# Optimization experiments

Measured on AMD Instinct MI355X. Metric: run time of the kernel, lower is better.

## Reference

```python
import jax, jax.numpy as jnp
import numpy as np
from jax import lax

B, S, D, F, T = 16, 1024, 256, 256, 8192
K = 3  # conv kernel size


def setup_inputs() -> dict:
    key = jax.random.key(0)
    ks = jax.random.split(key, 16)

    def conv_w(k, cin, cout):
        # kaiming-style, scaled down to keep exp(log_dur) in a sane range
        return jax.random.normal(k, (cout, cin, K), jnp.float32) * np.float32(np.sqrt(2.0 / (cin * K)) * 0.5)

    def lin_w(k, cin, cout, std=0.01):
        return jax.random.normal(k, (cin, cout), jnp.float32) * np.float32(std)

    inp = {
        "x": jax.random.normal(ks[0], (B, S, D), jnp.float32),
        "phone_masks": jnp.zeros((B, S), bool),
        "note_pitch": jax.random.normal(ks[1], (B, S, D), jnp.float32),
        # DurationPredictor (has extra LayerNorm)
        "ln_g": jnp.ones((D,), jnp.float32),
        "ln_b": jnp.zeros((D,), jnp.float32),
        "dp_w1": conv_w(ks[2], D, F), "dp_b1": jnp.full((F,), 0.1, jnp.float32),
        "dp_w2": conv_w(ks[3], F, F), "dp_b2": jnp.full((F,), 0.1, jnp.float32),
        "dp_wl": lin_w(ks[4], F, 1), "dp_bl": jnp.full((1,), 1.5, jnp.float32),
        # Pitch predictor (output_dim=3, bias [5.4, 1.7, 0.0])
        "pp_w1": conv_w(ks[5], D, F), "pp_b1": jnp.full((F,), 0.1, jnp.float32),
        "pp_w2": conv_w(ks[6], F, F), "pp_b2": jnp.full((F,), 0.1, jnp.float32),
        "pp_wl": lin_w(ks[7], F, 3), "pp_bl": jnp.array([5.4, 1.7, 0.0], jnp.float32),
        # Energy predictor (output_dim=1, bias 1.0)
        "ep_w1": conv_w(ks[8], D, F), "ep_b1": jnp.full((F,), 0.1, jnp.float32),
        "ep_w2": conv_w(ks[9], F, F), "ep_b2": jnp.full((F,), 0.1, jnp.float32),
        "ep_wl": lin_w(ks[10], F, 1), "ep_bl": jnp.full((1,), 1.0, jnp.float32),
        # note projection Linear(D, D)
        "np_w": lin_w(ks[11], D, D, std=1.0 / np.sqrt(D)),
        "np_b": jnp.zeros((D,), jnp.float32),
        "max_length": T,
    }
    return inp


def _conv1d(h, w, b):
    # h: [B, C, S], w: [O, C, K] -> [B, O, S], SAME padding (torch padding=(K-1)//2)
    y = lax.conv_general_dilated(h, w, (1,), "SAME", dimension_numbers=("NCH", "OIH", "NCH"))
    return y + b[None, :, None]


def _predictor(x, mask, w1, b1, w2, b2, wl, bl):
    # SimpleVariancePredictor.forward (dropout = eval-mode identity)
    h = jnp.swapaxes(x, 1, 2)                       # [B, C, S]
    h = jax.nn.relu(_conv1d(h, w1, b1))
    h = jax.nn.relu(_conv1d(h, w2, b2))
    out = jnp.swapaxes(h, 1, 2) @ wl + bl           # [B, S, out_dim]
    return jnp.where(mask[..., None], 0.0, out)


def _layernorm(x, g, b, eps=1e-5):
    m = jnp.mean(x, axis=-1, keepdims=True)
    v = jnp.mean(jnp.square(x - m), axis=-1, keepdims=True)
    return g * (x - m) * lax.rsqrt(v + eps) + b


def _duration_predictor(x, mask, ln_g, ln_b, w1, b1, w2, b2, wl, bl):
    xn = _layernorm(x, ln_g, ln_b)
    phoneme_energy = jnp.linalg.norm(xn, axis=2, keepdims=True)     # [B, S, 1]
    base = _predictor(xn, mask, w1, b1, w2, b2, wl, bl)
    energy_scale = 0.8 + 0.4 * (phoneme_energy / jnp.max(phoneme_energy))
    seq_len = x.shape[1]
    pos = jnp.arange(seq_len, dtype=x.dtype)[None, :, None]
    pos_scale = 1.0 + 0.1 * (pos / seq_len)
    out = base * energy_scale * pos_scale
    return jnp.where(mask[..., None], 0.0, out)


def _length_regulate(x, durations, max_length):
    # x: [B, S, C], durations: [B, S] float -> expanded [B, T, C], mel_masks [B, T]
    d = jnp.round(durations).astype(jnp.int32)
    cum = jnp.cumsum(d, axis=1)
    # _limit_durations: clip cumsum at max_length == reduce overflow token, zero the rest
    cumc = jnp.minimum(cum, max_length)
    t = jnp.arange(max_length, dtype=jnp.int32)
    # frame t belongs to phoneme j with cumc[j-1] <= t < cumc[j]  (parallel prefix-sum indexing)
    idx = jax.vmap(lambda c: jnp.searchsorted(c, t, side="right"))(cumc)   # [B, T]
    mel_masks = t[None, :] >= cumc[:, -1:]
    seq_len = x.shape[1]
    expanded = jnp.take_along_axis(x, jnp.clip(idx, 0, seq_len - 1)[:, :, None], axis=1)
    expanded = jnp.where(mel_masks[:, :, None], 0.0, expanded)
    return expanded, mel_masks


def reference(x, phone_masks, note_pitch, ln_g, ln_b,
              dp_w1, dp_b1, dp_w2, dp_b2, dp_wl, dp_bl,
              pp_w1, pp_b1, pp_w2, pp_b2, pp_wl, pp_bl,
              ep_w1, ep_b1, ep_w2, ep_b2, ep_wl, ep_bl,
              np_w, np_b, max_length):
    tempo_factor = 1.0
    x = x + (note_pitch @ np_w + np_b)

    log_durations = _duration_predictor(x, phone_masks, ln_g, ln_b,
                                        dp_w1, dp_b1, dp_w2, dp_b2, dp_wl, dp_bl)
    durations = jnp.exp(log_durations) * tempo_factor               # [B, S, 1]

    pitch_params = _predictor(x, phone_masks, pp_w1, pp_b1, pp_w2, pp_b2, pp_wl, pp_bl)  # [B, S, 3]
    phoneme_energy = jnp.linalg.norm(x, axis=2, keepdims=True)
    energy_norm = (phoneme_energy - jnp.min(phoneme_energy)) / (
        jnp.max(phoneme_energy) - jnp.min(phoneme_energy) + 1e-8)
    f0_scale = 100.0 + 400.0 * jnp.squeeze(energy_norm, -1)          # [B, S]
    f0_base = jnp.exp(pitch_params[:, :, 0]) * f0_scale / 220.0
    modified_f0 = jnp.log(f0_base + 1e-8)
    pitch_params = jnp.concatenate([modified_f0[..., None], pitch_params[:, :, 1:]], axis=2)

    energy = _predictor(x, phone_masks, ep_w1, ep_b1, ep_w2, ep_b2, ep_wl, ep_bl)        # [B, S, 1]

    expanded_features, mel_masks = _length_regulate(x, jnp.squeeze(durations, -1), max_length)
    return log_durations, durations, pitch_params, energy, expanded_features, mel_masks
```

## Files before the change

### kernel.cpp

```cpp
#include <hip/hip_runtime.h>
#include <math.h>

#define B_ 16
#define S_ 1024
#define D_ 256
#define F_ 256
#define T_ 8192
#define ROWS (B_ * S_)

typedef __attribute__((ext_vector_type(8))) short short8x;
typedef __attribute__((ext_vector_type(4))) float f32x4;

static __device__ __forceinline__ unsigned short f2bf(float f) {
    unsigned u = __float_as_uint(f);
    unsigned r = (u + 0x7FFFu + ((u >> 16) & 1u)) >> 16;
    return (unsigned short)r;
}
static __device__ __forceinline__ float bf2f(unsigned short h) {
    return __uint_as_float(((unsigned)h) << 16);
}

__global__ __launch_bounds__(256) void wprep_kernel(
    const float* __restrict__ pw1, const float* __restrict__ ew1,
    const float* __restrict__ pw2, const float* __restrict__ ew2,
    const float* __restrict__ dw1, const float* __restrict__ dw2,
    unsigned short* __restrict__ wt)
{
    int idx = blockIdx.x * 256 + threadIdx.x;
    int o = idx >> 8, c = idx & 255;
    int o_t = o >> 6, nt = (o >> 4) & 3, lr = o & 15;
    int cbk = c >> 5, hs = (c >> 3) & 3, j = c & 7;
    int lane = hs * 16 + lr;
    size_t fbase = ((size_t)o_t * 8 + cbk) * 3;

    const float* srcs[4] = { pw1, ew1, pw2, ew2 };
    #pragma unroll
    for (int t = 0; t < 4; ++t) {
        const float* p = srcs[t] + ((size_t)o * 256 + c) * 3;
        unsigned short* dst = wt + (size_t)t * 196608;
        #pragma unroll
        for (int k = 0; k < 3; ++k) {
            size_t off = (((fbase + k) * 4 + nt) * 64 + lane) * 8 + j;
            dst[off] = f2bf(p[k]);
        }
    }
    const float* dsrc[2] = { dw1, dw2 };
    #pragma unroll
    for (int t = 0; t < 2; ++t) {
        const float* p = dsrc[t] + ((size_t)o * 256 + c) * 3;
        unsigned short* dh = wt + (size_t)(4 + 2 * t) * 196608;
        unsigned short* dl = dh + 196608;
        #pragma unroll
        for (int k = 0; k < 3; ++k) {
            size_t off = (((fbase + k) * 4 + nt) * 64 + lane) * 8 + j;
            float v = p[k];
            unsigned short hi = f2bf(v);
            dh[off] = hi;
            dl[off] = f2bf(v - bf2f(hi));
        }
    }
}

__global__ __launch_bounds__(256) void noteproj_kernel(
    const float* __restrict__ x, const float* __restrict__ note,
    const float* __restrict__ w, const float* __restrict__ bias,
    float* __restrict__ xp, unsigned* __restrict__ red)
{
    if (blockIdx.x == 0 && blockIdx.y == 0 && threadIdx.x == 0) {
        red[0] = 0u;
        red[1] = 0x7F7FFFFFu;
        red[2] = 0u;
    }
    __shared__ float As[16][66];
    __shared__ float Bs[16][68];
    const int tid = threadIdx.x;
    const int m0 = blockIdx.x << 6;
    const int o0 = blockIdx.y << 6;
    const int tc = tid & 15, tr = tid >> 4;
    const int r = tr << 2, oc = tc << 2;
    const int tA = tid >> 2, cg = (tid & 3) << 2;
    const int cB = tid >> 4, oB = (tid & 15) << 2;
    float acc[4][4] = {};

    for (int c0 = 0; c0 < D_; c0 += 16) {
        float4 av = *(const float4*)(note + (size_t)(m0 + tA) * D_ + c0 + cg);
        As[cg + 0][tA] = av.x; As[cg + 1][tA] = av.y;
        As[cg + 2][tA] = av.z; As[cg + 3][tA] = av.w;
        *(float4*)&Bs[cB][oB] = *(const float4*)(w + (size_t)(c0 + cB) * D_ + o0 + oB);
        __syncthreads();
        #pragma unroll
        for (int c = 0; c < 16; ++c) {
            float a[4], bv[4];
            #pragma unroll
            for (int m = 0; m < 4; ++m) a[m] = As[c][r + m];
            #pragma unroll
            for (int j = 0; j < 4; ++j) bv[j] = Bs[c][oc + j];
            #pragma unroll
            for (int i = 0; i < 4; ++i)
                #pragma unroll
                for (int j = 0; j < 4; ++j)
                    acc[i][j] = fmaf(a[i], bv[j], acc[i][j]);
        }
        __syncthreads();
    }
    #pragma unroll
    for (int i = 0; i < 4; ++i) {
        size_t row = (size_t)(m0 + r + i);
        const float* xr = x + row * D_ + o0 + oc;
        float4 v;
        v.x = acc[i][0] + bias[o0 + oc + 0] + xr[0];
        v.y = acc[i][1] + bias[o0 + oc + 1] + xr[1];
        v.z = acc[i][2] + bias[o0 + oc + 2] + xr[2];
        v.w = acc[i][3] + bias[o0 + oc + 3] + xr[3];
        *(float4*)(xp + row * D_ + o0 + oc) = v;
    }
}

__global__ __launch_bounds__(256) void rowstats_kernel(
    const float* __restrict__ xp, const float* __restrict__ g, const float* __restrict__ bb,
    unsigned short* __restrict__ xnh, unsigned short* __restrict__ xnl,
    float* __restrict__ nxn, float* __restrict__ nx,
    unsigned short* __restrict__ xpb)
{
    int row = blockIdx.x * 4 + (threadIdx.x >> 6);
    int lane = threadIdx.x & 63;
    float4 v = ((const float4*)(xp + (size_t)row * D_))[lane];
    ushort4 bv4;
    bv4.x = f2bf(v.x); bv4.y = f2bf(v.y); bv4.z = f2bf(v.z); bv4.w = f2bf(v.w);
    ((ushort4*)xpb)[(size_t)row * 64 + lane] = bv4;

    float s = v.x + v.y + v.z + v.w;
    float sq = v.x * v.x + v.y * v.y + v.z * v.z + v.w * v.w;
    #pragma unroll
    for (int m = 32; m; m >>= 1) { s += __shfl_xor(s, m); sq += __shfl_xor(sq, m); }
    float mean = s * (1.f / 256.f);
    float var = sq * (1.f / 256.f) - mean * mean;
    float rs = rsqrtf(var + 1e-5f);
    float4 gv = ((const float4*)g)[lane];
    float4 bv = ((const float4*)bb)[lane];
    float4 o;
    o.x = gv.x * (v.x - mean) * rs + bv.x;
    o.y = gv.y * (v.y - mean) * rs + bv.y;
    o.z = gv.z * (v.z - mean) * rs + bv.z;
    o.w = gv.w * (v.w - mean) * rs + bv.w;
    ushort4 h4, l4;
    h4.x = f2bf(o.x); l4.x = f2bf(o.x - bf2f(h4.x));
    h4.y = f2bf(o.y); l4.y = f2bf(o.y - bf2f(h4.y));
    h4.z = f2bf(o.z); l4.z = f2bf(o.z - bf2f(h4.z));
    h4.w = f2bf(o.w); l4.w = f2bf(o.w - bf2f(h4.w));
    ((ushort4*)xnh)[(size_t)row * 64 + lane] = h4;
    ((ushort4*)xnl)[(size_t)row * 64 + lane] = l4;

    float q = o.x * o.x + o.y * o.y + o.z * o.z + o.w * o.w;
    #pragma unroll
    for (int m = 32; m; m >>= 1) q += __shfl_xor(q, m);
    if (lane == 0) { nxn[row] = sqrtf(q); nx[row] = sqrtf(sq); }
}

__global__ __launch_bounds__(256) void reduce_fast_kernel(
    const float* __restrict__ nxn, const float* __restrict__ nx, unsigned* __restrict__ red)
{
    int tid = threadIdx.x;
    int lane = tid & 63, wave = tid >> 6;
    float mxn = 0.f, mnx = 3.0e38f, mxx = 0.f;
    for (int i = blockIdx.x * 256 + tid; i < ROWS; i += 32 * 256) {
        mxn = fmaxf(mxn, nxn[i]);
        float v = nx[i];
        mnx = fminf(mnx, v);
        mxx = fmaxf(mxx, v);
    }
    #pragma unroll
    for (int m = 32; m; m >>= 1) {
        mxn = fmaxf(mxn, __shfl_xor(mxn, m));
        mnx = fminf(mnx, __shfl_xor(mnx, m));
        mxx = fmaxf(mxx, __shfl_xor(mxx, m));
    }
    __shared__ float a0[4], a1[4], a2[4];
    if (lane == 0) { a0[wave] = mxn; a1[wave] = mnx; a2[wave] = mxx; }
    __syncthreads();
    if (tid == 0) {
        #pragma unroll
        for (int w2 = 1; w2 < 4; ++w2) {
            mxn = fmaxf(mxn, a0[w2]); mnx = fminf(mnx, a1[w2]); mxx = fmaxf(mxx, a2[w2]);
        }
        atomicMax(&red[0], __float_as_uint(mxn));
        atomicMin(&red[1], __float_as_uint(mnx));
        atomicMax(&red[2], __float_as_uint(mxx));
    }
}

struct ConvAll {
    const unsigned short* dp_in_hi; const unsigned short* dp_in_lo;
    const unsigned short* dp_wt_hi; const unsigned short* dp_wt_lo;
    const float* dp_bias;
    unsigned short* dp_out_hi; unsigned short* dp_out_lo;
    float* dp_out_f;
    const unsigned short* inb[2];
    const unsigned short* wt[2];
    const float* bias[2];
    void* out[2];
    int bfout;
};

__global__ __launch_bounds__(256) void convall_kernel(ConvAll cb)
{
    __shared__ __align__(16) char smem[36864];
    const int tid = threadIdx.x;
    const int z = blockIdx.z;
    const int o0 = blockIdx.y << 6;
    const int wave = tid >> 6, lane = tid & 63;
    const int lm = lane & 15, lk8 = (lane >> 4) << 3;
    const int q4 = (lane >> 4) << 2;

    if (z == 0) {
        if (blockIdx.x >= 64) return;
        const int b = blockIdx.x >> 2;
        const int S0 = (blockIdx.x & 3) << 8;
        const int wr = wave << 6;
        f32x4 acc[4][4] = {};
        unsigned aoff[4][3]; bool aok[4][3];
        #pragma unroll
        for (int st = 0; st < 4; ++st)
            #pragma unroll
            for (int k = 0; k < 3; ++k) {
                int srow = S0 + wr + (st << 4) + lm + k - 1;
                aok[st][k] = (srow >= 0) && (srow < S_);
                int sr = srow < 0 ? 0 : (srow >= S_ ? S_ - 1 : srow);
                aoff[st][k] = (unsigned)(b * S_ + sr) * D_ + lk8;
            }
        const unsigned short* ih = cb.dp_in_hi;
        const unsigned short* il = cb.dp_in_lo;
        const unsigned short* wh = cb.dp_wt_hi + (size_t)(o0 >> 6) * 49152 + (size_t)lane * 8;
        const unsigned short* wl = cb.dp_wt_lo + (size_t)(o0 >> 6) * 49152 + (size_t)lane * 8;
        for (int c0 = 0; c0 < D_; c0 += 32) {
            const int cbi = c0 >> 5;
            #pragma unroll
            for (int k = 0; k < 3; ++k) {
                uint4 ah4[4], al4[4];
                #pragma unroll
                for (int st = 0; st < 4; ++st) {
                    uint4 vh = make_uint4(0u, 0u, 0u, 0u);
                    uint4 vl = make_uint4(0u, 0u, 0u, 0u);
                    if (aok[st][k]) {
                        unsigned off = aoff[st][k] + c0;
                        vh = *(const uint4*)(const void*)(ih + off);
                        vl = *(const uint4*)(const void*)(il + off);
                    }
                    ah4[st] = vh; al4[st] = vl;
                }
                const unsigned short* bph = wh + (size_t)((cbi * 3 + k) * 4) * 512;
                const unsigned short* bpl = wl + (size_t)((cbi * 3 + k) * 4) * 512;
                #pragma unroll
                for (int nt = 0; nt < 4; ++nt) {
                    short8x bh = *(const short8x*)(const void*)(bph + nt * 512);
                    short8x bl = *(const short8x*)(const void*)(bpl + nt * 512);
                    #pragma unroll
                    for (int st = 0; st < 4; ++st) {
                        short8x ah = *(short8x*)&ah4[st];
                        short8x al = *(short8x*)&al4[st];
                        acc[st][nt] = __builtin_amdgcn_mfma_f32_16x16x32_bf16(ah, bh, acc[st][nt], 0, 0, 0);
                        acc[st][nt] = __builtin_amdgcn_mfma_f32_16x16x32_bf16(ah, bl, acc[st][nt], 0, 0, 0);
                        acc[st][nt] = __builtin_amdgcn_mfma_f32_16x16x32_bf16(al, bh, acc[st][nt], 0, 0, 0);
                    }
                }
            }
        }
        float bvv[4];
        #pragma unroll
        for (int nt = 0; nt < 4; ++nt) bvv[nt] = cb.dp_bias[o0 + (nt << 4) + lm];
        const int hw = wr >> 7;
        const int base = wr & 127;
        if (cb.bfout) {
            unsigned short* L = (unsigned short*)smem;
            #pragma unroll
            for (int pass = 0; pass < 2; ++pass) {
                unsigned short* outp = pass ? cb.dp_out_lo : cb.dp_out_hi;
                #pragma unroll
                for (int h = 0; h < 2; ++h) {
                    if (pass | h) __syncthreads();
                    if (hw == h) {
                        #pragma unroll
                        for (int nt = 0; nt < 4; ++nt)
                            #pragma unroll
                            for (int st = 0; st < 4; ++st)
                                #pragma unroll
                                for (int rg = 0; rg < 4; ++rg) {
                                    int lrow = base + (st << 4) + q4 + rg;
                                    int lcol = (nt << 4) + lm;
                                    float v = fmaxf(acc[st][nt][rg] + bvv[nt], 0.f);
                                    unsigned short hi = f2bf(v);
                                    L[lrow * 72 + lcol] = pass ? f2bf(v - bf2f(hi)) : hi;
                                }
                    }
                    __syncthreads();
                    #pragma unroll
                    for (int q = 0; q < 4; ++q) {
                        int flat = (q << 8) + tid;
                        int rrow = flat >> 3, u = flat & 7;
                        uint4 val = *(const uint4*)(const void*)&L[rrow * 72 + (u << 3)];
                        *(uint4*)(void*)(outp + ((size_t)(b * S_ + S0 + (h << 7) + rrow)) * D_ + o0 + (u << 3)) = val;
                    }
                }
            }
        } else {
            float* Lf = (float*)smem;
            #pragma unroll
            for (int h = 0; h < 2; ++h) {
                if (h) __syncthreads();
                if (hw == h) {
                    #pragma unroll
                    for (int nt = 0; nt < 4; ++nt)
                        #pragma unroll
                        for (int st = 0; st < 4; ++st)
                            #pragma unroll
                            for (int rg = 0; rg < 4; ++rg) {
                                int lrow = base + (st << 4) + q4 + rg;
                                int lcol = (nt << 4) + lm;
                                Lf[lrow * 72 + lcol] = fmaxf(acc[st][nt][rg] + bvv[nt], 0.f);
                            }
                }
                __syncthreads();
                #pragma unroll
                for (int q = 0; q < 8; ++q) {
                    int flat = (q << 8) + tid;
                    int rrow = flat >> 4, u4 = flat & 15;
                    uint4 val = *(const uint4*)(const void*)&Lf[rrow * 72 + (u4 << 2)];
                    *(uint4*)(void*)(cb.dp_out_f + ((size_t)(b * S_ + S0 + (h << 7) + rrow)) * D_ + o0 + (u4 << 2)) = val;
                }
            }
        }
    } else {
        if (blockIdx.x >= 64) return;
        const int z1 = z - 1;
        const int b = blockIdx.x >> 2;
        const int S0 = (blockIdx.x & 3) << 8;
        const int wr = wave << 6;
        f32x4 acc[4][4] = {};
        unsigned aoff[4][3]; bool aok[4][3];
        #pragma unroll
        for (int st = 0; st < 4; ++st)
            #pragma unroll
            for (int k = 0; k < 3; ++k) {
                int srow = S0 + wr + (st << 4) + lm + k - 1;
                aok[st][k] = (srow >= 0) && (srow < S_);
                int sr = srow < 0 ? 0 : (srow >= S_ ? S_ - 1 : srow);
                aoff[st][k] = (unsigned)(b * S_ + sr) * D_ + lk8;
            }
        const unsigned short* inp = cb.inb[z1];
        const unsigned short* wp = cb.wt[z1] + (size_t)(o0 >> 6) * 49152 + (size_t)lane * 8;
        for (int c0 = 0; c0 < D_; c0 += 32) {
            const int cbi = c0 >> 5;
            uint4 pa[4][3];
            #pragma unroll
            for (int st = 0; st < 4; ++st)
                #pragma unroll
                for (int k = 0; k < 3; ++k) {
                    uint4 v = make_uint4(0u, 0u, 0u, 0u);
                    if (aok[st][k]) v = *(const uint4*)(const void*)(inp + aoff[st][k] + c0);
                    pa[st][k] = v;
                }
            #pragma unroll
            for (int k = 0; k < 3; ++k) {
                const unsigned short* bp = wp + (size_t)((cbi * 3 + k) * 4) * 512;
                short8x a0 = *(short8x*)&pa[0][k];
                short8x a1 = *(short8x*)&pa[1][k];
                short8x a2 = *(short8x*)&pa[2][k];
                short8x a3 = *(short8x*)&pa[3][k];
                #pragma unroll
                for (int nt = 0; nt < 4; ++nt) {
                    short8x bf = *(const short8x*)(const void*)(bp + nt * 512);
                    acc[0][nt] = __builtin_amdgcn_mfma_f32_16x16x32_bf16(a0, bf, acc[0][nt], 0, 0, 0);
                    acc[1][nt] = __builtin_amdgcn_mfma_f32_16x16x32_bf16(a1, bf, acc[1][nt], 0, 0, 0);
                    acc[2][nt] = __builtin_amdgcn_mfma_f32_16x16x32_bf16(a2, bf, acc[2][nt], 0, 0, 0);
                    acc[3][nt] = __builtin_amdgcn_mfma_f32_16x16x32_bf16(a3, bf, acc[3][nt], 0, 0, 0);
                }
            }
        }
        float bvv[4];
        #pragma unroll
        for (int nt = 0; nt < 4; ++nt) bvv[nt] = cb.bias[z1][o0 + (nt << 4) + lm];
        const int hw = wr >> 7;
        const int base = wr & 127;
        if (cb.bfout) {
            unsigned short* L = (unsigned short*)smem;
            unsigned short* outp = (unsigned short*)cb.out[z1];
            #pragma unroll
            for (int h = 0; h < 2; ++h) {
                if (h) __syncthreads();
                if (hw == h) {
                    #pragma unroll
                    for (int nt = 0; nt < 4; ++nt)
                        #pragma unroll
                        for (int st = 0; st < 4; ++st)
                            #pragma unroll
                            for (int rg = 0; rg < 4; ++rg) {
                                int lrow = base + (st << 4) + q4 + rg;
                                int lcol = (nt << 4) + lm;
                                L[lrow * 72 + lcol] = f2bf(fmaxf(acc[st][nt][rg] + bvv[nt], 0.f));
                            }
                }
                __syncthreads();
                #pragma unroll
                for (int q = 0; q < 4; ++q) {
                    int flat = (q << 8) + tid;
                    int rrow = flat >> 3, u = flat & 7;
                    uint4 val = *(const uint4*)(const void*)&L[rrow * 72 + (u << 3)];
                    *(uint4*)(void*)(outp + ((size_t)(b * S_ + S0 + (h << 7) + rrow)) * D_ + o0 + (u << 3)) = val;
                }
            }
        } else {
            float* Lf = (float*)smem;
            float* outp = (float*)cb.out[z1];
            #pragma unroll
            for (int h = 0; h < 2; ++h) {
                if (h) __syncthreads();
                if (hw == h) {
                    #pragma unroll
                    for (int nt = 0; nt < 4; ++nt)
                        #pragma unroll
                        for (int st = 0; st < 4; ++st)
                            #pragma unroll
                            for (int rg = 0; rg < 4; ++rg) {
                                int lrow = base + (st << 4) + q4 + rg;
                                int lcol = (nt << 4) + lm;
                                Lf[lrow * 72 + lcol] = fmaxf(acc[st][nt][rg] + bvv[nt], 0.f);
                            }
                }
                __syncthreads();
                #pragma unroll
                for (int q = 0; q < 8; ++q) {
                    int flat = (q << 8) + tid;
                    int rrow = flat >> 4, u4 = flat & 15;
                    uint4 val = *(const uint4*)(const void*)&Lf[rrow * 72 + (u4 << 2)];
                    *(uint4*)(void*)(outp + ((size_t)(b * S_ + S0 + (h << 7) + rrow)) * D_ + o0 + (u4 << 2)) = val;
                }
            }
        }
    }
}

__global__ __launch_bounds__(256) void linfused_kernel(
    const float* __restrict__ h2dp, const float* __restrict__ h2pp, const float* __restrict__ h2ep,
    const float* __restrict__ dp_wl, const float* __restrict__ dp_bl,
    const float* __restrict__ pp_wl, const float* __restrict__ pp_bl,
    const float* __restrict__ ep_wl, const float* __restrict__ ep_bl,
    const float* __restrict__ nxn, const float* __restrict__ nx, const unsigned* __restrict__ red,
    float* __restrict__ o_logdur, float* __restrict__ o_dur, float* __restrict__ durf,
    float* __restrict__ o_pitch, float* __restrict__ o_energy)
{
    int row = blockIdx.x * 4 + (threadIdx.x >> 6);
    int lane = threadIdx.x & 63;
    float4 hd = ((const float4*)(h2dp + (size_t)row * F_))[lane];
    float4 wd = ((const float4*)dp_wl)[lane];
    float ad = hd.x * wd.x + hd.y * wd.y + hd.z * wd.z + hd.w * wd.w;

    float4 he = ((const float4*)(h2ep + (size_t)row * F_))[lane];
    float4 we = ((const float4*)ep_wl)[lane];
    float ae = he.x * we.x + he.y * we.y + he.z * we.z + he.w * we.w;

    float4 hp = ((const float4*)(h2pp + (size_t)row * F_))[lane];
    float hv[4] = { hp.x, hp.y, hp.z, hp.w };
    float a0 = 0.f, a1 = 0.f, a2 = 0.f;
    #pragma unroll
    for (int u = 0; u < 4; ++u) {
        int c = lane * 4 + u;
        a0 = fmaf(hv[u], pp_wl[c * 3 + 0], a0);
        a1 = fmaf(hv[u], pp_wl[c * 3 + 1], a1);
        a2 = fmaf(hv[u], pp_wl[c * 3 + 2], a2);
    }
    #pragma unroll
    for (int m = 32; m; m >>= 1) {
        ad += __shfl_xor(ad, m);
        ae += __shfl_xor(ae, m);
        a0 += __shfl_xor(a0, m); a1 += __shfl_xor(a1, m); a2 += __shfl_xor(a2, m);
    }
    if (lane == 0) {
        float base = ad + dp_bl[0];
        float es = 0.8f + 0.4f * (nxn[row] / __uint_as_float(red[0]));
        int s = row & (S_ - 1);
        float ps = 1.0f + 0.1f * ((float)s * (1.f / (float)S_));
        float ld = base * es * ps;
        float d = expf(ld);
        o_logdur[row] = ld;
        o_dur[row] = d;
        durf[row] = d;
        float p0 = a0 + pp_bl[0], p1 = a1 + pp_bl[1], p2 = a2 + pp_bl[2];
        float mn = __uint_as_float(red[1]), mx = __uint_as_float(red[2]);
        float en = (nx[row] - mn) / (mx - mn + 1e-8f);
        float f0s = 100.f + 400.f * en;
        float f0b = expf(p0) * f0s * (1.f / 220.f);
        o_pitch[(size_t)row * 3 + 0] = logf(f0b + 1e-8f);
        o_pitch[(size_t)row * 3 + 1] = p1;
        o_pitch[(size_t)row * 3 + 2] = p2;
        o_energy[row] = ae + ep_bl[0];
    }
}

__global__ __launch_bounds__(1024) void regulate_kernel(
    const float* __restrict__ durf, int* __restrict__ idxbuf, float* __restrict__ mask)
{
    __shared__ int cum[S_];
    int b = blockIdx.x;
    int t = threadIdx.x;
    int d = (int)rintf(durf[b * S_ + t]);
    cum[t] = d;
    __syncthreads();
    for (int off = 1; off < S_; off <<= 1) {
        int v = (t >= off) ? cum[t - off] : 0;
        __syncthreads();
        cum[t] += v;
        __syncthreads();
    }
    cum[t] = min(cum[t], T_);
    __syncthreads();
    int total = cum[S_ - 1];
    for (int t0 = t; t0 < T_; t0 += S_) {
        int lo = 0, hi = S_;
        while (lo < hi) {
            int mid = (lo + hi) >> 1;
            if (cum[mid] <= t0) lo = mid + 1; else hi = mid;
        }
        int id = min(lo, S_ - 1);
        bool masked = (t0 >= total);
        idxbuf[b * T_ + t0] = masked ? -1 : id;
        mask[(size_t)b * T_ + t0] = masked ? 1.f : 0.f;
    }
}

__global__ __launch_bounds__(256) void expand_kernel(
    const float* __restrict__ xp, const int* __restrict__ idxbuf, float* __restrict__ expd)
{
    int row = blockIdx.x * 4 + (threadIdx.x >> 6);
    int lane = threadIdx.x & 63;
    int id = idxbuf[row];
    int b = row >> 13;
    float4 v = make_float4(0.f, 0.f, 0.f, 0.f);
    if (id >= 0)
        v = ((const float4*)(xp + ((size_t)(b * S_ + id)) * D_))[lane];
    ((float4*)(expd + (size_t)row * D_))[lane] = v;
}

extern "C" void kernel_launch(void* const* d_in, const int* in_sizes, int n_in,
                              void* d_out, int out_size, void* d_ws, size_t ws_size,
                              hipStream_t stream) {
    const float* x     = (const float*)d_in[0];
    const float* note  = (const float*)d_in[2];
    const float* ln_g  = (const float*)d_in[3];
    const float* ln_b  = (const float*)d_in[4];
    const float* dp_w1 = (const float*)d_in[5];
    const float* dp_b1 = (const float*)d_in[6];
    const float* dp_w2 = (const float*)d_in[7];
    const float* dp_b2 = (const float*)d_in[8];
    const float* dp_wl = (const float*)d_in[9];
    const float* dp_bl = (const float*)d_in[10];
    const float* pp_w1 = (const float*)d_in[11];
    const float* pp_b1 = (const float*)d_in[12];
    const float* pp_w2 = (const float*)d_in[13];
    const float* pp_b2 = (const float*)d_in[14];
    const float* pp_wl = (const float*)d_in[15];
    const float* pp_bl = (const float*)d_in[16];
    const float* ep_w1 = (const float*)d_in[17];
    const float* ep_b1 = (const float*)d_in[18];
    const float* ep_w2 = (const float*)d_in[19];
    const float* ep_b2 = (const float*)d_in[20];
    const float* ep_wl = (const float*)d_in[21];
    const float* ep_bl = (const float*)d_in[22];
    const float* np_w  = (const float*)d_in[23];
    const float* np_b  = (const float*)d_in[24];

    float* o_logdur = (float*)d_out;
    float* o_dur    = o_logdur + ROWS;
    float* o_pitch  = o_dur + ROWS;
    float* o_energy = o_pitch + ROWS * 3;
    float* o_exp    = o_energy + ROWS;
    float* o_mask   = o_exp + (size_t)B_ * T_ * D_;

    const size_t CH = (size_t)ROWS * D_;
    float* h2_dp = o_exp + 0 * CH;
    float* h2_pp = o_exp + 1 * CH;
    float* h2_ep = o_exp + 2 * CH;
    unsigned short* h1_ppb  = (unsigned short*)(o_exp + 3 * CH);
    unsigned short* h1_epb  = (unsigned short*)(o_exp + 3 * CH + CH / 2);
    unsigned short* xp_bf   = (unsigned short*)(o_exp + 4 * CH);
    unsigned short* xn_hi   = (unsigned short*)(o_exp + 4 * CH + CH / 2);
    unsigned short* xn_lo   = (unsigned short*)(o_exp + 5 * CH);
    unsigned short* h1dp_hi = (unsigned short*)(o_exp + 5 * CH + CH / 2);
    unsigned short* h1dp_lo = (unsigned short*)(o_exp + 6 * CH);
    unsigned short* wt      = (unsigned short*)(o_exp + 6 * CH + CH / 2);
    unsigned short* wt_pp1  = wt;
    unsigned short* wt_ep1  = wt + 196608;
    unsigned short* wt_pp2  = wt + 2 * 196608;
    unsigned short* wt_ep2  = wt + 3 * 196608;
    unsigned short* wt_dp1h = wt + 4 * 196608;
    unsigned short* wt_dp1l = wt + 5 * 196608;
    unsigned short* wt_dp2h = wt + 6 * 196608;
    unsigned short* wt_dp2l = wt + 7 * 196608;

    float* ws_f    = (float*)d_ws;
    float* xprime  = ws_f;
    float* norm_xn = ws_f + CH;
    float* norm_x  = norm_xn + ROWS;
    unsigned* red  = (unsigned*)(norm_x + ROWS);
    float* durf    = (float*)(red + 4);
    int*   idxbuf  = (int*)(durf + ROWS);

    wprep_kernel<<<256, 256, 0, stream>>>(pp_w1, ep_w1, pp_w2, ep_w2, dp_w1, dp_w2, wt);
    noteproj_kernel<<<dim3(ROWS / 64, D_ / 64), 256, 0, stream>>>(x, note, np_w, np_b, xprime, red);
    rowstats_kernel<<<ROWS / 4, 256, 0, stream>>>(xprime, ln_g, ln_b, xn_hi, xn_lo, norm_xn, norm_x, xp_bf);
    reduce_fast_kernel<<<32, 256, 0, stream>>>(norm_xn, norm_x, red);

    dim3 cgrid(B_ * (S_ / 128), F_ / 64, 3);
    ConvAll s1;
    s1.dp_in_hi = xn_hi;   s1.dp_in_lo = xn_lo;
    s1.dp_wt_hi = wt_dp1h; s1.dp_wt_lo = wt_dp1l;
    s1.dp_bias = dp_b1;
    s1.dp_out_hi = h1dp_hi; s1.dp_out_lo = h1dp_lo; s1.dp_out_f = nullptr;
    s1.inb[0] = xp_bf;  s1.wt[0] = wt_pp1; s1.bias[0] = pp_b1; s1.out[0] = (void*)h1_ppb;
    s1.inb[1] = xp_bf;  s1.wt[1] = wt_ep1; s1.bias[1] = ep_b1; s1.out[1] = (void*)h1_epb;
    s1.bfout = 1;
    convall_kernel<<<cgrid, 256, 0, stream>>>(s1);

    ConvAll s2;
    s2.dp_in_hi = h1dp_hi; s2.dp_in_lo = h1dp_lo;
    s2.dp_wt_hi = wt_dp2h; s2.dp_wt_lo = wt_dp2l;
    s2.dp_bias = dp_b2;
    s2.dp_out_hi = nullptr; s2.dp_out_lo = nullptr; s2.dp_out_f = h2_dp;
    s2.inb[0] = h1_ppb; s2.wt[0] = wt_pp2; s2.bias[0] = pp_b2; s2.out[0] = (void*)h2_pp;
    s2.inb[1] = h1_epb; s2.wt[1] = wt_ep2; s2.bias[1] = ep_b2; s2.out[1] = (void*)h2_ep;
    s2.bfout = 0;
    convall_kernel<<<cgrid, 256, 0, stream>>>(s2);

    linfused_kernel<<<ROWS / 4, 256, 0, stream>>>(h2_dp, h2_pp, h2_ep,
        dp_wl, dp_bl, pp_wl, pp_bl, ep_wl, ep_bl,
        norm_xn, norm_x, red, o_logdur, o_dur, durf, o_pitch, o_energy);

    regulate_kernel<<<B_, 1024, 0, stream>>>(durf, idxbuf, o_mask);
    expand_kernel<<<(B_ * T_) / 4, 256, 0, stream>>>(xprime, idxbuf, o_exp);
}
```

Baseline: 404.5 us.

## Move note projection GEMM onto bf16 MFMA with hi/lo split precision

Replaces the scalar FP32 shared-memory tiled note-projection GEMM with an MFMA kernel that uses three bf16x3 products (hi*hi, hi*lo, lo*hi) to keep close-to-fp32 accuracy. The weights are pre-split into hi/lo bf16 tiles in the existing weight-prep kernel. Activations are converted on the fly from global memory without LDS staging, and LDS is used only to transpose the output for coalesced residual add and store. This trades three MFMAs per tile and per-element conversions for far higher matrix throughput, but uses fewer blocks (256), which may limit occupancy.

```diff
diff --git a/kernel.cpp b/kernel.cpp
--- a/kernel.cpp
+++ b/kernel.cpp
@@ -24,6 +24,7 @@
     const float* __restrict__ pw1, const float* __restrict__ ew1,
     const float* __restrict__ pw2, const float* __restrict__ ew2,
     const float* __restrict__ dw1, const float* __restrict__ dw2,
+    const float* __restrict__ npw,
     unsigned short* __restrict__ wt)
 {
     int idx = blockIdx.x * 256 + threadIdx.x;
@@ -59,11 +60,21 @@
             dl[off] = f2bf(v - bf2f(hi));
         }
     }
-}
-
-__global__ __launch_bounds__(256) void noteproj_kernel(
-    const float* __restrict__ x, const float* __restrict__ note,
-    const float* __restrict__ w, const float* __restrict__ bias,
+    {
+        float v = npw[(size_t)c * 256 + o];
+        unsigned short hi = f2bf(v);
+        size_t off2 = (((size_t)(o_t * 8 + cbk) * 4 + nt) * 64 + lane) * 8 + j;
+        unsigned short* nh = wt + (size_t)8 * 196608;
+        unsigned short* nl = nh + 65536;
+        nh[off2] = hi;
+        nl[off2] = f2bf(v - bf2f(hi));
+    }
+}
+
+__global__ __launch_bounds__(256) void noteproj_mfma_kernel(
+    const float* __restrict__ note,
+    const unsigned short* __restrict__ wh, const unsigned short* __restrict__ wl,
+    const float* __restrict__ x, const float* __restrict__ bias,
     float* __restrict__ xp, unsigned* __restrict__ red)
 {
     if (blockIdx.x == 0 && blockIdx.y == 0 && threadIdx.x == 0) {
@@ -71,48 +82,83 @@
         red[1] = 0x7F7FFFFFu;
         red[2] = 0u;
     }
-    __shared__ float As[16][66];
-    __shared__ float Bs[16][68];
+    __shared__ __align__(16) char smem[36864];
     const int tid = threadIdx.x;
-    const int m0 = blockIdx.x << 6;
     const int o0 = blockIdx.y << 6;
-    const int tc = tid & 15, tr = tid >> 4;
-    const int r = tr << 2, oc = tc << 2;
-    const int tA = tid >> 2, cg = (tid & 3) << 2;
-    const int cB = tid >> 4, oB = (tid & 15) << 2;
-    float acc[4][4] = {};
-
-    for (int c0 = 0; c0 < D_; c0 += 16) {
-        float4 av = *(const float4*)(note + (size_t)(m0 + tA) * D_ + c0 + cg);
-        As[cg + 0][tA] = av.x; As[cg + 1][tA] = av.y;
-        As[cg + 2][tA] = av.z; As[cg + 3][tA] = av.w;
-        *(float4*)&Bs[cB][oB] = *(const float4*)(w + (size_t)(c0 + cB) * D_ + o0 + oB);
+    const int R0 = blockIdx.x << 8;
+    const int wave = tid >> 6, lane = tid & 63;
+    const int lm = lane & 15, lk8 = (lane >> 4) << 3;
+    const int q4 = (lane >> 4) << 2;
+    const int wr = wave << 6;
+    f32x4 acc[4][4] = {};
+    unsigned aoff[4];
+    #pragma unroll
+    for (int st = 0; st < 4; ++st)
+        aoff[st] = (unsigned)(R0 + wr + (st << 4) + lm) * D_ + lk8;
+    const unsigned short* whp = wh + (size_t)(o0 >> 6) * 16384 + (size_t)lane * 8;
+    const unsigned short* wlp = wl + (size_t)(o0 >> 6) * 16384 + (size_t)lane * 8;
+    for (int c0 = 0; c0 < D_; c0 += 32) {
+        const int cbi = c0 >> 5;
+        short8x ah[4], al[4];
+        #pragma unroll
+        for (int st = 0; st < 4; ++st) {
+            float4 va = *(const float4*)(note + aoff[st] + c0);
+            float4 vb = *(const float4*)(note + aoff[st] + c0 + 4);
+            float vv[8] = { va.x, va.y, va.z, va.w, vb.x, vb.y, vb.z, vb.w };
+            #pragma unroll
+            for (int e = 0; e < 8; ++e) {
+                unsigned short hi = f2bf(vv[e]);
+                ah[st][e] = (short)hi;
+                al[st][e] = (short)f2bf(vv[e] - bf2f(hi));
+            }
+        }
+        const unsigned short* bph = whp + (size_t)(cbi * 4) * 512;
+        const unsigned short* bpl = wlp + (size_t)(cbi * 4) * 512;
+        #pragma unroll
+        for (int nt = 0; nt < 4; ++nt) {
+            short8x bh = *(const short8x*)(const void*)(bph + nt * 512);
+            short8x bl = *(const short8x*)(const void*)(bpl + nt * 512);
+            #pragma unroll
+            for (int st = 0; st < 4; ++st) {
+                acc[st][nt] = __builtin_amdgcn_mfma_f32_16x16x32_bf16(ah[st], bh, acc[st][nt], 0, 0, 0);
+                acc[st][nt] = __builtin_amdgcn_mfma_f32_16x16x32_bf16(ah[st], bl, acc[st][nt], 0, 0, 0);
+                acc[st][nt] = __builtin_amdgcn_mfma_f32_16x16x32_bf16(al[st], bh, acc[st][nt], 0, 0, 0);
+            }
+        }
+    }
+    float bvv[4];
+    #pragma unroll
+    for (int nt = 0; nt < 4; ++nt) bvv[nt] = bias[o0 + (nt << 4) + lm];
+    const int hw = wr >> 7, base = wr & 127;
+    float* Lf = (float*)smem;
+    #pragma unroll
+    for (int h = 0; h < 2; ++h) {
+        if (h) __syncthreads();
+        if (hw == h) {
+            #pragma unroll
+            for (int nt = 0; nt < 4; ++nt)
+                #pragma unroll
+                for (int st = 0; st < 4; ++st)
+                    #pragma unroll
+                    for (int rg = 0; rg < 4; ++rg) {
+                        int lrow = base + (st << 4) + q4 + rg;
+                        int lcol = (nt << 4) + lm;
+                        Lf[lrow * 72 + lcol] = acc[st][nt][rg] + bvv[nt];
+                    }
+        }
         __syncthreads();
         #pragma unroll
-        for (int c = 0; c < 16; ++c) {
-            float a[4], bv[4];
-            #pragma unroll
-            for (int m = 0; m < 4; ++m) a[m] = As[c][r + m];
-            #pragma unroll
-            for (int j = 0; j < 4; ++j) bv[j] = Bs[c][oc + j];
-            #pragma unroll
-            for (int i = 0; i < 4; ++i)
-                #pragma unroll
-                for (int j = 0; j < 4; ++j)
-                    acc[i][j] = fmaf(a[i], bv[j], acc[i][j]);
-        }
-        __syncthreads();
-    }
-    #pragma unroll
-    for (int i = 0; i < 4; ++i) {
-        size_t row = (size_t)(m0 + r + i);
-        const float* xr = x + row * D_ + o0 + oc;
-        float4 v;
-        v.x = acc[i][0] + bias[o0 + oc + 0] + xr[0];
-        v.y = acc[i][1] + bias[o0 + oc + 1] + xr[1];
-        v.z = acc[i][2] + bias[o0 + oc + 2] + xr[2];
-        v.w = acc[i][3] + bias[o0 + oc + 3] + xr[3];
-        *(float4*)(xp + row * D_ + o0 + oc) = v;
+        for (int q = 0; q < 8; ++q) {
+            int flat = (q << 8) + tid;
+            int rrow = flat >> 4, u4 = flat & 15;
+            size_t off = ((size_t)(R0 + (h << 7) + rrow)) * D_ + o0 + (u4 << 2);
+            float4 lv = *(const float4*)(const void*)&Lf[rrow * 72 + (u4 << 2)];
+            float4 xv = *(const float4*)(x + off);
+            float4 ov;
+            ov.x = lv.x + xv.x; ov.y = lv.y + xv.y;
+            ov.z = lv.z + xv.z; ov.w = lv.w + xv.w;
+            *(float4*)(xp + off) = ov;
+        }
     }
 }
 
@@ -595,6 +641,8 @@
     unsigned short* wt_dp1l = wt + 5 * 196608;
     unsigned short* wt_dp2h = wt + 6 * 196608;
     unsigned short* wt_dp2l = wt + 7 * 196608;
+    unsigned short* wt_nph  = wt + 8 * 196608;
+    unsigned short* wt_npl  = wt_nph + 65536;
 
     float* ws_f    = (float*)d_ws;
     float* xprime  = ws_f;
@@ -604,8 +652,8 @@
     float* durf    = (float*)(red + 4);
     int*   idxbuf  = (int*)(durf + ROWS);
 
-    wprep_kernel<<<256, 256, 0, stream>>>(pp_w1, ep_w1, pp_w2, ep_w2, dp_w1, dp_w2, wt);
-    noteproj_kernel<<<dim3(ROWS / 64, D_ / 64), 256, 0, stream>>>(x, note, np_w, np_b, xprime, red);
+    wprep_kernel<<<256, 256, 0, stream>>>(pp_w1, ep_w1, pp_w2, ep_w2, dp_w1, dp_w2, np_w, wt);
+    noteproj_mfma_kernel<<<dim3(64, 4), 256, 0, stream>>>(note, wt_nph, wt_npl, x, np_b, xprime, red);
     rowstats_kernel<<<ROWS / 4, 256, 0, stream>>>(xprime, ln_g, ln_b, xn_hi, xn_lo, norm_xn, norm_x, xp_bf);
     reduce_fast_kernel<<<32, 256, 0, stream>>>(norm_xn, norm_x, red);
 
```

New measurement: 409.5 us. Within noise of the previous version (+1.2%).
